# Kernel tuning notes

Measured on AMD Instinct MI355X. Metric: run time of the kernel, lower is better.

Reference implementation:

```python
import jax, jax.numpy as jnp
import numpy as np

B, C, H, W = 16, 512, 112, 112
OUT, GMM = 8, 4
SIGMA_RATIO = 1.0
R = 3.0
BN_EPS = 1e-5


def conv3(x, w):
    # 3x3 conv, stride 1, padding 1 (SAME), NCHW / OIHW
    return jax.lax.conv_general_dilated(x, w, (1, 1), 'SAME',
                                        dimension_numbers=('NCHW', 'OIHW', 'NCHW'))


def bn_relu(x, g, b):
    # inference-mode BatchNorm2d (running_mean=0, running_var=1) + ReLU
    s = g / jnp.sqrt(1.0 + BN_EPS)
    return jax.nn.relu(x * s[None, :, None, None] + b[None, :, None, None])


def setup_inputs() -> dict:
    key = jax.random.key(0)
    ks = jax.random.split(key, 20)
    def w(k, shape, s=0.05):
        return jax.random.normal(k, shape, dtype=jnp.float32) * s
    inp = {
        'x':  jax.random.normal(ks[0], (B, C, H, W), dtype=jnp.float32),
        'w1': w(ks[1], (C // 2, C, 3, 3)),
        'g1': 1.0 + w(ks[2], (C // 2,), 0.1), 'b1': w(ks[3], (C // 2,), 0.1),
        'w2': w(ks[4], (C // 2, C // 2, 3, 3)),
        'g2': 1.0 + w(ks[5], (C // 2,), 0.1), 'b2': w(ks[6], (C // 2,), 0.1),
        'w3': w(ks[7], (C // 4, C // 2, 3, 3)),
        'g3': 1.0 + w(ks[8], (C // 4,), 0.1), 'b3': w(ks[9], (C // 4,), 0.1),
        'w4': w(ks[10], (C // 4, C // 4, 3, 3)),
        'g4': 1.0 + w(ks[11], (C // 4,), 0.1), 'b4': w(ks[12], (C // 4,), 0.1),
        'w5': w(ks[13], (C // 8, C // 4, 3, 3)),
        'g5': 1.0 + w(ks[14], (C // 8,), 0.1), 'b5': w(ks[15], (C // 8,), 0.1),
        'w_fc': w(ks[16], (4 * GMM * OUT, 9 * C // 8)),
        'mix_w': jnp.zeros((1, OUT, GMM, 1, 1), dtype=jnp.float32),
    }
    return inp


def reference(x, w1, g1, b1, w2, g2, b2, w3, g3, b3, w4, g4, b4, w5, g5, b5,
              w_fc, mix_w):
    Bn, Cn, Hh, Ww = x.shape
    h = bn_relu(conv3(x, w1), g1, b1)
    h = bn_relu(conv3(h, w2), g2, b2)
    # AdaptiveAvgPool2d((7,7)): 112/7 = 16, exact reshape-mean
    h = h.reshape(Bn, Cn // 2, 7, Hh // 7, 7, Ww // 7).mean(axis=(3, 5))
    h = bn_relu(conv3(h, w3), g3, b3)
    h = bn_relu(conv3(h, w4), g4, b4)
    # AdaptiveAvgPool2d((3,3)) on 7x7: overlapping windows size 3, stride 2
    h = jax.lax.reduce_window(h, 0.0, jax.lax.add, (1, 1, 3, 3), (1, 1, 2, 2), 'VALID') / 9.0
    h = bn_relu(conv3(h, w5), g5, b5)        # [B, C/8, 3, 3]
    feats = h.reshape(Bn, -1) @ w_fc.T       # [B, 4*gmm*out]
    f = feats.reshape(Bn, OUT, GMM, 4)

    H2, W2 = Hh // 2, Ww // 2
    m_x = jax.nn.sigmoid(f[..., 0]) * float(H2 - 1)           # [B,out,gmm]
    m_y = jax.nn.sigmoid(f[..., 1]) * float(W2 - 1)
    r = jnp.exp((jax.nn.sigmoid(f[..., 2]) * 2.0 - 1.0) * np.float32(np.log(R)))
    rho = jax.nn.sigmoid(f[..., 3]) * 1.6 - 0.8
    sigma = float(Hh) / (2.0 * SIGMA_RATIO)
    denom = -0.5 / (1.0 - rho ** 2) / (sigma ** 2)            # [B,out,gmm]

    ii = jnp.arange(H2, dtype=x.dtype)
    jj = jnp.arange(W2, dtype=x.dtype)
    dx = m_x[..., None] - ii   # [B,out,gmm,H2]
    dy = m_y[..., None] - jj   # [B,out,gmm,W2]
    quad = (dx ** 2 * r[..., None])[..., :, None] \
         + (dy ** 2 / r[..., None])[..., None, :] \
         - 2.0 * rho[..., None, None] * dx[..., :, None] * dy[..., None, :]
    att = jnp.exp(denom[..., None, None] * quad)              # [B,out,gmm,H2,W2]
    att = att / att.sum(axis=(3, 4), keepdims=True)
    mw = jax.nn.softmax(mix_w, axis=2)                        # [1,out,gmm,1,1]
    return (att * mw).sum(axis=2)                             # [B,out,H2,W2]
```

## Files before the change

### kernel.cpp

```cpp
#include <hip/hip_runtime.h>
#include <math.h>


typedef __attribute__((ext_vector_type(8))) short short8v;
typedef __attribute__((ext_vector_type(4))) float f32x4;

__device__ __forceinline__ void split_bf16(float f, unsigned int& hi, unsigned int& lo)
{
    unsigned int u = __float_as_uint(f);
    hi = u >> 16;
    float hif = __uint_as_float(u & 0xffff0000u);
    lo = __float_as_uint(f - hif) >> 16;
}

__device__ __forceinline__ void gld16(const void* g, void* l)
{
    __builtin_amdgcn_global_load_lds(
        (const __attribute__((address_space(1))) unsigned int*)g,
        (__attribute__((address_space(3))) unsigned int*)l, 16, 0, 0);
}

__global__ void zero_kernel(float* z) { z[threadIdx.x] = 0.f; }

__global__ __launch_bounds__(256)
void prep_w_kernel(const float* __restrict__ w, unsigned short* __restrict__ wp, int CIN)
{
    int idx = blockIdx.x * 256 + threadIdx.x;
    int NCH = CIN >> 5;
    int total = 2 * NCH * 9 * 2 * 128 * 32;
    if (idx >= total) return;
    int kk = idx & 31;
    int co = (idx >> 5) & 127;
    int pl = (idx >> 12) & 1;
    int rest = idx >> 13;
    int tap = rest % 9;
    rest /= 9;
    int ch = rest % NCH;
    int y = rest / NCH;
    int qp = kk >> 3, e = kk & 7;
    int q = qp ^ ((co >> 1) & 3);
    int ci = ch * 32 + q * 8 + e;
    int cog = y * 128 + co;
    float f = w[((size_t)cog * CIN + ci) * 9 + tap];
    unsigned int hi, lo;
    split_bf16(f, hi, lo);
    wp[idx] = (unsigned short)(pl ? lo : hi);
}

__global__ __launch_bounds__(256)
void presplit_x_kernel(const float* __restrict__ x, unsigned short* __restrict__ xs)
{
    const int gy = blockIdx.x, ch = blockIdx.y, b = blockIdx.z;
    const int tid = threadIdx.x;
    __shared__ float s[32][113];
    for (int i = tid; i < 32 * 112; i += 256) {
        int ci = i / 112, xx = i - ci * 112;
        s[ci][xx] = x[(((size_t)(b * 16 + ch) * 32 + ci) * 112 + gy) * 112 + xx];
    }
    __syncthreads();
    unsigned int* oh = (unsigned int*)(xs + ((size_t)(b * 16 + ch) * 2 * 12544 + (size_t)gy * 112) * 32);
    unsigned int* ol = oh + 12544 * 16;
    for (int i = tid; i < 112 * 16; i += 256) {
        int px = i >> 4, t = i & 15;
        int qp = t >> 2, ep = t & 3;
        int sw = ((18 * gy + px + 19) >> 1) & 3;
        int q = qp ^ sw;
        int ci0 = q * 8 + ep * 2;
        float f0 = s[ci0][px], f1 = s[ci0 + 1][px];
        unsigned int h0, l0, h1, l1;
        split_bf16(f0, h0, l0);
        split_bf16(f1, h1, l1);
        oh[(size_t)px * 16 + t] = h0 | (h1 << 16);
        ol[(size_t)px * 16 + t] = l0 | (l1 << 16);
    }
}

template<int CIN, bool POOL>
__global__ __launch_bounds__(256, 2)
void conv_mfma_kernel(const unsigned short* __restrict__ xs,
                      const unsigned short* __restrict__ wp,
                      const float* __restrict__ gam, const float* __restrict__ bet,
                      void* __restrict__ out_, const float* __restrict__ zerob)
{
    constexpr int NCH = CIN >> 5;
    extern __shared__ __align__(16) char smem[];
    char* sA = smem;
    char* sB = smem + 43008;

    const int tid = threadIdx.x;
    const int lane = tid & 63;
    const int wv = tid >> 6;
    const int wvm = wv >> 1, ng = wv & 1;
    const int m = lane & 15, kg = lane >> 4;
    const int ty = blockIdx.x / 7, tx = blockIdx.x % 7;
    const int yb = blockIdx.y;
    const int b = blockIdx.z;

    int aoff[11];
    unsigned adst[11];
    #pragma unroll
    for (int k2 = 0; k2 < 11; ++k2) {
        int j = wv + 4 * k2;
        aoff[k2] = -1; adst[k2] = 0;
        if (j < 42) {
            int pl = j / 21, jj = j - pl * 21;
            int px = jj * 16 + (lane >> 2);
            int py = px / 18, pxx = px - py * 18;
            int gy = ty * 16 + py - 1, gx = tx * 16 + pxx - 1;
            bool valid = (px < 324) && ((unsigned)gy < 112u) && ((unsigned)gx < 112u);
            aoff[k2] = valid ? (pl * 802816 + ((gy * 112 + gx) << 6) + ((lane & 3) << 4)) : -1;
            adst[k2] = pl * 21504 + jj * 1024;
        }
    }
    const char* zb = (const char*)zerob + ((lane & 3) << 4);

    auto issueA = [&](int ch) {
        const char* xbase = (const char*)xs + (size_t)(b * NCH + ch) * 1605632;
        #pragma unroll
        for (int k2 = 0; k2 < 11; ++k2) {
            if (wv + 4 * k2 < 42) {
                const char* g = (aoff[k2] >= 0) ? (xbase + aoff[k2]) : zb;
                gld16(g, sA + adst[k2]);
            }
        }
    };
    const char* wbase = (const char*)wp + (size_t)yb * ((size_t)NCH * 9 * 16384);
    auto issueB = [&](int flat, int half) {
        const char* gb = wbase + (size_t)flat * 16384 + (wv << 12) + (lane << 4);
        char* db = sB + half * 16384 + (wv << 12);
        #pragma unroll
        for (int j2 = 0; j2 < 4; ++j2)
            gld16(gb + j2 * 1024, db + j2 * 1024);
    };

    f32x4 acc[8][4];
    #pragma unroll
    for (int i = 0; i < 8; ++i)
        #pragma unroll
        for (int j = 0; j < 4; ++j)
            acc[i][j] = (f32x4){0.f, 0.f, 0.f, 0.f};

    auto mfma_tap = [&](int tap, const char* sBc) {
        const int ky = tap / 3, kx = tap % 3;
        short8v Bf[8];
        #pragma unroll
        for (int nf = 0; nf < 4; ++nf) {
            int col = ng * 64 + nf * 16 + m;
            int off = col * 64 + ((kg ^ ((col >> 1) & 3)) << 4);
            Bf[nf * 2 + 0] = *(const short8v*)(sBc + off);
            Bf[nf * 2 + 1] = *(const short8v*)(sBc + 8192 + off);
        }
        #pragma unroll
        for (int mf = 0; mf < 8; ++mf) {
            int ap = (wvm * 8 + mf + ky) * 18 + kx + m;
            int off = ap * 64 + ((kg ^ ((ap >> 1) & 3)) << 4);
            short8v Ah = *(const short8v*)(sA + off);
            short8v Al = *(const short8v*)(sA + 21504 + off);
            #pragma unroll
            for (int nf = 0; nf < 4; ++nf) {
                acc[mf][nf] = __builtin_amdgcn_mfma_f32_16x16x32_bf16(Ah, Bf[nf * 2 + 0], acc[mf][nf], 0, 0, 0);
                acc[mf][nf] = __builtin_amdgcn_mfma_f32_16x16x32_bf16(Ah, Bf[nf * 2 + 1], acc[mf][nf], 0, 0, 0);
                acc[mf][nf] = __builtin_amdgcn_mfma_f32_16x16x32_bf16(Al, Bf[nf * 2 + 0], acc[mf][nf], 0, 0, 0);
            }
        }
    };

    issueA(0);
    issueB(0, 0);
    issueB(1, 1);
    asm volatile("s_waitcnt vmcnt(0)" ::: "memory");
    __syncthreads();

    for (int ch = 0; ch < NCH; ++ch) {
        const int base = ch * 9;
        #pragma unroll
        for (int pe = 0; pe < 4; ++pe) {
            mfma_tap(2 * pe, sB);
            mfma_tap(2 * pe + 1, sB + 16384);
            __syncthreads();
            if (pe < 3) {
                issueB(base + 2 * pe + 2, 0);
                issueB(base + 2 * pe + 3, 1);
            } else {
                issueB(base + 8, 0);
            }
            asm volatile("s_waitcnt vmcnt(0)" ::: "memory");
            __syncthreads();
        }
        mfma_tap(8, sB);
        __syncthreads();
        if (ch + 1 < NCH) {
            issueA(ch + 1);
            issueB(base + 9, 0);
            issueB(base + 10, 1);
        }
        asm volatile("s_waitcnt vmcnt(0)" ::: "memory");
        __syncthreads();
    }

    const float kRS = 1.0f / sqrtf(1.0f + 1e-5f);

    if (!POOL) {
        unsigned short* h1s = (unsigned short*)out_;
        #pragma unroll
        for (int mf = 0; mf < 8; ++mf) {
            int gy = ty * 16 + wvm * 8 + mf;
            #pragma unroll
            for (int nf = 0; nf < 4; ++nf) {
                int co = yb * 128 + ng * 64 + nf * 16 + m;
                float sc = gam[co] * kRS, bi = bet[co];
                int ch2 = co >> 5, sl = co & 31, q = sl >> 3, e = sl & 7;
                size_t base2 = (size_t)(b * 8 + ch2) * 802816;
                #pragma unroll
                for (int r = 0; r < 4; ++r) {
                    int gx = tx * 16 + kg * 4 + r;
                    float v = fmaxf(fmaf(acc[mf][nf][r], sc, bi), 0.f);
                    unsigned int hi, lo;
                    split_bf16(v, hi, lo);
                    int sw = ((18 * gy + gx + 19) >> 1) & 3;
                    size_t po = base2 + ((size_t)gy * 112 + gx) * 32 + (size_t)((q ^ sw) * 8 + e);
                    h1s[po] = (unsigned short)hi;
                    h1s[po + 401408] = (unsigned short)lo;
                }
            }
        }
    } else {
        __syncthreads();
        float* spool = (float*)sA;
        #pragma unroll
        for (int nf = 0; nf < 4; ++nf) {
            int co = yb * 128 + ng * 64 + nf * 16 + m;
            float sc = gam[co] * kRS, bi = bet[co];
            float s = 0.f;
            #pragma unroll
            for (int mf = 0; mf < 8; ++mf)
                #pragma unroll
                for (int r = 0; r < 4; ++r)
                    s += fmaxf(fmaf(acc[mf][nf][r], sc, bi), 0.f);
            s += __shfl_xor(s, 16);
            s += __shfl_xor(s, 32);
            if (lane < 16) spool[(wv * 4 + nf) * 16 + lane] = s;
        }
        __syncthreads();
        if (tid < 128) {
            int ngx = tid >> 6, rem = tid & 63;
            int nf = rem >> 4, mm = rem & 15;
            float s = spool[(ngx * 4 + nf) * 16 + mm] + spool[((2 + ngx) * 4 + nf) * 16 + mm];
            float* p1o = (float*)out_;
            p1o[(((size_t)b * 256 + yb * 128 + tid) * 7 + ty) * 7 + tx] = s * (1.f / 256.f);
        }
    }
}


template<int CIN>
__global__ __launch_bounds__(256)
void conv_small_kernel(const float* __restrict__ in, const float* __restrict__ w,
                       const float* __restrict__ gam, const float* __restrict__ bet,
                       float* __restrict__ out, int CO_TOT)
{
    const int co0 = blockIdx.x * 16;
    const int b = blockIdx.y;
    const int tid = threadIdx.x;
    const int px = tid & 63;
    const int wg = tid >> 6;
    const int py = px / 7, pxx = px - py * 7;
    const bool act = px < 49;

    __shared__ float s_in[64][9][9];
    __shared__ float s_w[64][16][9];

    float acc[4] = {0.f, 0.f, 0.f, 0.f};

    for (int ci0 = 0; ci0 < CIN; ci0 += 64) {
        __syncthreads();
        for (int idx = tid; idx < 64 * 81; idx += 256) {
            int ci = idx / 81;
            int rem = idx - ci * 81;
            int r = rem / 9, c = rem - (rem / 9) * 9;
            float v = 0.f;
            if (r >= 1 && r <= 7 && c >= 1 && c <= 7)
                v = in[((size_t)(b * CIN + ci0 + ci) * 7 + (r - 1)) * 7 + (c - 1)];
            s_in[ci][r][c] = v;
        }
        for (int idx = tid; idx < 64 * 16 * 9; idx += 256) {
            int co = idx / 576;
            int rem = idx - co * 576;
            int ci = rem / 9, tap = rem - (rem / 9) * 9;
            s_w[ci][co][tap] = w[((size_t)(co0 + co) * CIN + ci0 + ci) * 9 + tap];
        }
        __syncthreads();
        if (act) {
            for (int ci = 0; ci < 64; ++ci) {
                #pragma unroll
                for (int ky = 0; ky < 3; ++ky)
                    #pragma unroll
                    for (int kx = 0; kx < 3; ++kx) {
                        float v = s_in[ci][py + ky][pxx + kx];
                        #pragma unroll
                        for (int j = 0; j < 4; ++j)
                            acc[j] = fmaf(v, s_w[ci][wg * 4 + j][ky * 3 + kx], acc[j]);
                    }
            }
        }
    }
    if (act) {
        const float kRS = 1.0f / sqrtf(1.0f + 1e-5f);
        #pragma unroll
        for (int j = 0; j < 4; ++j) {
            int cog = co0 + wg * 4 + j;
            float v = fmaxf(fmaf(acc[j], gam[cog] * kRS, bet[cog]), 0.f);
            out[(size_t)(b * CO_TOT + cog) * 49 + py * 7 + pxx] = v;
        }
    }
}

__global__ void pool3x3_kernel(const float* __restrict__ in, float* __restrict__ out)
{
    int o = blockIdx.x * 256 + threadIdx.x;
    if (o >= 16 * 128 * 9) return;
    int xo = o % 3;
    int yo = (o / 3) % 3;
    int bc = o / 9;
    const float* p = in + (size_t)bc * 49;
    float s = 0.f;
    #pragma unroll
    for (int ky = 0; ky < 3; ++ky)
        #pragma unroll
        for (int kx = 0; kx < 3; ++kx)
            s += p[(yo * 2 + ky) * 7 + xo * 2 + kx];
    out[o] = s * (1.0f / 9.0f);
}

__global__ __launch_bounds__(256)
void conv5_kernel(const float* __restrict__ in, const float* __restrict__ w,
                  const float* __restrict__ gam, const float* __restrict__ bet,
                  float* __restrict__ out)
{
    const int co0 = blockIdx.x * 16;
    const int b = blockIdx.y;
    const int tid = threadIdx.x;
    __shared__ float s_in[128][5][5];
    __shared__ float s_w[64][16][9];

    for (int idx = tid; idx < 128 * 25; idx += 256) {
        int ci = idx / 25;
        int rem = idx - ci * 25;
        int r = rem / 5, c = rem - (rem / 5) * 5;
        float v = 0.f;
        if (r >= 1 && r <= 3 && c >= 1 && c <= 3)
            v = in[((size_t)(b * 128 + ci) * 3 + (r - 1)) * 3 + (c - 1)];
        s_in[ci][r][c] = v;
    }

    float acc = 0.f;
    const int co = tid / 9;
    const int px = tid - co * 9;
    const int pyy = px / 3, pxx = px - pyy * 3;
    const bool act = tid < 144;

    for (int ci0 = 0; ci0 < 128; ci0 += 64) {
        __syncthreads();
        for (int idx = tid; idx < 64 * 16 * 9; idx += 256) {
            int c2 = idx / 576;
            int rem = idx - c2 * 576;
            int ci = rem / 9, tap = rem - (rem / 9) * 9;
            s_w[ci][c2][tap] = w[((size_t)(co0 + c2) * 128 + ci0 + ci) * 9 + tap];
        }
        __syncthreads();
        if (act) {
            for (int ci = 0; ci < 64; ++ci) {
                #pragma unroll
                for (int ky = 0; ky < 3; ++ky)
                    #pragma unroll
                    for (int kx = 0; kx < 3; ++kx)
                        acc = fmaf(s_in[ci0 + ci][pyy + ky][pxx + kx],
                                   s_w[ci][co][ky * 3 + kx], acc);
            }
        }
    }
    if (act) {
        const float kRS = 1.0f / sqrtf(1.0f + 1e-5f);
        int cog = co0 + co;
        out[(size_t)(b * 64 + cog) * 9 + px] =
            fmaxf(fmaf(acc, gam[cog] * kRS, bet[cog]), 0.f);
    }
}

__global__ void fc_kernel(const float* __restrict__ h5, const float* __restrict__ wfc,
                          float* __restrict__ feats)
{
    int o = blockIdx.x * 256 + threadIdx.x;
    if (o >= 16 * 128) return;
    int b = o >> 7, j = o & 127;
    const float* hp = h5 + b * 576;
    const float* wp = wfc + j * 576;
    float s = 0.f;
    for (int k = 0; k < 576; ++k) s = fmaf(hp[k], wp[k], s);
    feats[o] = s;
}

__global__ __launch_bounds__(256)
void attn_kernel(const float* __restrict__ feats, const float* __restrict__ mixw,
                 float* __restrict__ out)
{
    const int bo = blockIdx.x;
    const int b = bo >> 3, o = bo & 7;
    const int tid = threadIdx.x;
    __shared__ float s_att[4][3136];
    __shared__ float s_red[4];

    float mv[4];
    float mmax = -1e30f;
    #pragma unroll
    for (int g = 0; g < 4; ++g) { mv[g] = mixw[o * 4 + g]; mmax = fmaxf(mmax, mv[g]); }
    float msum = 0.f;
    #pragma unroll
    for (int g = 0; g < 4; ++g) { mv[g] = expf(mv[g] - mmax); msum += mv[g]; }
    #pragma unroll
    for (int g = 0; g < 4; ++g) mv[g] /= msum;

    const float LOG_R = 1.0986122886681098f;
    float winv[4];
    for (int g = 0; g < 4; ++g) {
        float f0 = feats[b * 128 + o * 16 + g * 4 + 0];
        float f1 = feats[b * 128 + o * 16 + g * 4 + 1];
        float f2 = feats[b * 128 + o * 16 + g * 4 + 2];
        float f3 = feats[b * 128 + o * 16 + g * 4 + 3];
        float m_x = 55.f / (1.f + expf(-f0));
        float m_y = 55.f / (1.f + expf(-f1));
        float r = expf((2.f / (1.f + expf(-f2)) - 1.f) * LOG_R);
        float rho = 1.6f / (1.f + expf(-f3)) - 0.8f;
        float denom = (-0.5f / (1.f - rho * rho)) * (1.f / 3136.f);
        float rin = 1.f / r;

        float ssum = 0.f;
        for (int p = tid; p < 3136; p += 256) {
            int i = p / 56;
            int j = p - i * 56;
            float dx = m_x - (float)i;
            float dy = m_y - (float)j;
            float quad = dx * dx * r + dy * dy * rin - 2.f * rho * dx * dy;
            float e = expf(denom * quad);
            s_att[g][p] = e;
            ssum += e;
        }
        #pragma unroll
        for (int off = 32; off > 0; off >>= 1) ssum += __shfl_down(ssum, off);
        if ((tid & 63) == 0) s_red[tid >> 6] = ssum;
        __syncthreads();
        winv[g] = mv[g] / (s_red[0] + s_red[1] + s_red[2] + s_red[3]);
        __syncthreads();
    }

    for (int p = tid; p < 3136; p += 256) {
        float v = 0.f;
        #pragma unroll
        for (int g = 0; g < 4; ++g) v += s_att[g][p] * winv[g];
        out[(size_t)bo * 3136 + p] = v;
    }
}


extern "C" void kernel_launch(void* const* d_in, const int* in_sizes, int n_in,
                              void* d_out, int out_size, void* d_ws, size_t ws_size,
                              hipStream_t stream)
{
    const float* x    = (const float*)d_in[0];
    const float* w1   = (const float*)d_in[1];
    const float* g1   = (const float*)d_in[2];
    const float* b1   = (const float*)d_in[3];
    const float* w2   = (const float*)d_in[4];
    const float* g2   = (const float*)d_in[5];
    const float* b2   = (const float*)d_in[6];
    const float* w3   = (const float*)d_in[7];
    const float* g3   = (const float*)d_in[8];
    const float* b3   = (const float*)d_in[9];
    const float* w4   = (const float*)d_in[10];
    const float* g4   = (const float*)d_in[11];
    const float* b4   = (const float*)d_in[12];
    const float* w5   = (const float*)d_in[13];
    const float* g5   = (const float*)d_in[14];
    const float* b5   = (const float*)d_in[15];
    const float* wfc  = (const float*)d_in[16];
    const float* mixw = (const float*)d_in[17];
    float* outp = (float*)d_out;

    hipFuncSetAttribute(reinterpret_cast<const void*>(&conv_mfma_kernel<512, false>),
                        hipFuncAttributeMaxDynamicSharedMemorySize, 75776);
    hipFuncSetAttribute(reinterpret_cast<const void*>(&conv_mfma_kernel<256, true>),
                        hipFuncAttributeMaxDynamicSharedMemorySize, 75776);

    char* wsb = (char*)d_ws;
    unsigned short* wp = (unsigned short*)wsb;   wsb += (size_t)2359296 * 2;
    unsigned short* xs = (unsigned short*)wsb;   wsb += (size_t)16*16*2*12544*32*2;
    unsigned short* h1s = (unsigned short*)wsb;  wsb += (size_t)16*8*2*12544*32*2;
    float* p1 = (float*)wsb;  wsb += 200704 * 4;
    float* h3 = (float*)wsb;  wsb += 100352 * 4;
    float* h4 = (float*)wsb;  wsb += 100352 * 4;
    float* p2 = (float*)wsb;  wsb += 18432 * 4;
    float* h5 = (float*)wsb;  wsb += 9216 * 4;
    float* fts = (float*)wsb; wsb += 2048 * 4;
    float* zerob = (float*)wsb; wsb += 64 * 4;

    zero_kernel<<<1, 64, 0, stream>>>(zerob);
    presplit_x_kernel<<<dim3(112, 16, 16), 256, 0, stream>>>(x, xs);

    prep_w_kernel<<<9216, 256, 0, stream>>>(w1, wp, 512);
    conv_mfma_kernel<512, false><<<dim3(49, 2, 16), 256, 75776, stream>>>(xs, wp, g1, b1, h1s, zerob);

    prep_w_kernel<<<4608, 256, 0, stream>>>(w2, wp, 256);
    conv_mfma_kernel<256, true><<<dim3(49, 2, 16), 256, 75776, stream>>>(h1s, wp, g2, b2, p1, zerob);

    conv_small_kernel<256><<<dim3(8, 16), 256, 0, stream>>>(p1, w3, g3, b3, h3, 128);
    conv_small_kernel<128><<<dim3(8, 16), 256, 0, stream>>>(h3, w4, g4, b4, h4, 128);

    pool3x3_kernel<<<72, 256, 0, stream>>>(h4, p2);
    conv5_kernel<<<dim3(4, 16), 256, 0, stream>>>(p2, w5, g5, b5, h5);
    fc_kernel<<<8, 256, 0, stream>>>(h5, wfc, fts);
    attn_kernel<<<128, 256, 0, stream>>>(fts, mixw, outp);
}
```

Measured before the change: 1.912 ms.

## Store conv1 output as single bf16 and drop low-part MFMAs in conv2

```diff
diff --git a/kernel.cpp b/kernel.cpp
--- a/kernel.cpp
+++ b/kernel.cpp
@@ -83,9 +83,13 @@
                       void* __restrict__ out_, const float* __restrict__ zerob)
 {
     constexpr int NCH = CIN >> 5;
+    constexpr int APL = POOL ? 1 : 2;
+    constexpr int AJ = 21 * APL;
+    constexpr int AISS = (AJ + 3) / 4;
+    constexpr size_t XSTR = (size_t)802816 * APL;
     extern __shared__ __align__(16) char smem[];
     char* sA = smem;
-    char* sB = smem + 43008;
+    char* sB = smem + APL * 21504;
 
     const int tid = threadIdx.x;
     const int lane = tid & 63;
@@ -96,13 +100,13 @@
     const int yb = blockIdx.y;
     const int b = blockIdx.z;
 
-    int aoff[11];
-    unsigned adst[11];
-    #pragma unroll
-    for (int k2 = 0; k2 < 11; ++k2) {
+    int aoff[AISS];
+    unsigned adst[AISS];
+    #pragma unroll
+    for (int k2 = 0; k2 < AISS; ++k2) {
         int j = wv + 4 * k2;
         aoff[k2] = -1; adst[k2] = 0;
-        if (j < 42) {
+        if (j < AJ) {
             int pl = j / 21, jj = j - pl * 21;
             int px = jj * 16 + (lane >> 2);
             int py = px / 18, pxx = px - py * 18;
@@ -115,10 +119,10 @@
     const char* zb = (const char*)zerob + ((lane & 3) << 4);
 
     auto issueA = [&](int ch) {
-        const char* xbase = (const char*)xs + (size_t)(b * NCH + ch) * 1605632;
-        #pragma unroll
-        for (int k2 = 0; k2 < 11; ++k2) {
-            if (wv + 4 * k2 < 42) {
+        const char* xbase = (const char*)xs + (size_t)(b * NCH + ch) * XSTR;
+        #pragma unroll
+        for (int k2 = 0; k2 < AISS; ++k2) {
+            if (wv + 4 * k2 < AJ) {
                 const char* g = (aoff[k2] >= 0) ? (xbase + aoff[k2]) : zb;
                 gld16(g, sA + adst[k2]);
             }
@@ -142,25 +146,33 @@
 
     auto mfma_tap = [&](int tap, const char* sBc) {
         const int ky = tap / 3, kx = tap % 3;
-        short8v Bf[8];
+        short8v Bh_[4], Bl_[4];
         #pragma unroll
         for (int nf = 0; nf < 4; ++nf) {
             int col = ng * 64 + nf * 16 + m;
             int off = col * 64 + ((kg ^ ((col >> 1) & 3)) << 4);
-            Bf[nf * 2 + 0] = *(const short8v*)(sBc + off);
-            Bf[nf * 2 + 1] = *(const short8v*)(sBc + 8192 + off);
+            Bh_[nf] = *(const short8v*)(sBc + off);
+            Bl_[nf] = *(const short8v*)(sBc + 8192 + off);
         }
         #pragma unroll
         for (int mf = 0; mf < 8; ++mf) {
             int ap = (wvm * 8 + mf + ky) * 18 + kx + m;
             int off = ap * 64 + ((kg ^ ((ap >> 1) & 3)) << 4);
             short8v Ah = *(const short8v*)(sA + off);
-            short8v Al = *(const short8v*)(sA + 21504 + off);
-            #pragma unroll
-            for (int nf = 0; nf < 4; ++nf) {
-                acc[mf][nf] = __builtin_amdgcn_mfma_f32_16x16x32_bf16(Ah, Bf[nf * 2 + 0], acc[mf][nf], 0, 0, 0);
-                acc[mf][nf] = __builtin_amdgcn_mfma_f32_16x16x32_bf16(Ah, Bf[nf * 2 + 1], acc[mf][nf], 0, 0, 0);
-                acc[mf][nf] = __builtin_amdgcn_mfma_f32_16x16x32_bf16(Al, Bf[nf * 2 + 0], acc[mf][nf], 0, 0, 0);
+            if constexpr (!POOL) {
+                short8v Al = *(const short8v*)(sA + 21504 + off);
+                #pragma unroll
+                for (int nf = 0; nf < 4; ++nf) {
+                    acc[mf][nf] = __builtin_amdgcn_mfma_f32_16x16x32_bf16(Ah, Bh_[nf], acc[mf][nf], 0, 0, 0);
+                    acc[mf][nf] = __builtin_amdgcn_mfma_f32_16x16x32_bf16(Ah, Bl_[nf], acc[mf][nf], 0, 0, 0);
+                    acc[mf][nf] = __builtin_amdgcn_mfma_f32_16x16x32_bf16(Al, Bh_[nf], acc[mf][nf], 0, 0, 0);
+                }
+            } else {
+                #pragma unroll
+                for (int nf = 0; nf < 4; ++nf) {
+                    acc[mf][nf] = __builtin_amdgcn_mfma_f32_16x16x32_bf16(Ah, Bh_[nf], acc[mf][nf], 0, 0, 0);
+                    acc[mf][nf] = __builtin_amdgcn_mfma_f32_16x16x32_bf16(Ah, Bl_[nf], acc[mf][nf], 0, 0, 0);
+                }
             }
         }
     };
@@ -210,23 +222,22 @@
                 int co = yb * 128 + ng * 64 + nf * 16 + m;
                 float sc = gam[co] * kRS, bi = bet[co];
                 int ch2 = co >> 5, sl = co & 31, q = sl >> 3, e = sl & 7;
-                size_t base2 = (size_t)(b * 8 + ch2) * 802816;
+                size_t base2 = (size_t)(b * 8 + ch2) * 401408;
                 #pragma unroll
                 for (int r = 0; r < 4; ++r) {
                     int gx = tx * 16 + kg * 4 + r;
                     float v = fmaxf(fmaf(acc[mf][nf][r], sc, bi), 0.f);
-                    unsigned int hi, lo;
-                    split_bf16(v, hi, lo);
+                    unsigned int u = __float_as_uint(v);
+                    u += 0x7fffu + ((u >> 16) & 1u);
                     int sw = ((18 * gy + gx + 19) >> 1) & 3;
                     size_t po = base2 + ((size_t)gy * 112 + gx) * 32 + (size_t)((q ^ sw) * 8 + e);
-                    h1s[po] = (unsigned short)hi;
-                    h1s[po + 401408] = (unsigned short)lo;
+                    h1s[po] = (unsigned short)(u >> 16);
                 }
             }
         }
     } else {
         __syncthreads();
-        float* spool = (float*)sA;
+        float* spool = (float*)smem;
         #pragma unroll
         for (int nf = 0; nf < 4; ++nf) {
             int co = yb * 128 + ng * 64 + nf * 16 + m;
@@ -387,17 +398,20 @@
     }
 }
 
-__global__ void fc_kernel(const float* __restrict__ h5, const float* __restrict__ wfc,
-                          float* __restrict__ feats)
-{
-    int o = blockIdx.x * 256 + threadIdx.x;
-    if (o >= 16 * 128) return;
+__global__ __launch_bounds__(256)
+void fc_kernel(const float* __restrict__ h5, const float* __restrict__ wfc,
+               float* __restrict__ feats)
+{
+    int o = blockIdx.x * 4 + (threadIdx.x >> 6);
+    int lane = threadIdx.x & 63;
     int b = o >> 7, j = o & 127;
     const float* hp = h5 + b * 576;
     const float* wp = wfc + j * 576;
     float s = 0.f;
-    for (int k = 0; k < 576; ++k) s = fmaf(hp[k], wp[k], s);
-    feats[o] = s;
+    for (int k = lane; k < 576; k += 64) s = fmaf(hp[k], wp[k], s);
+    #pragma unroll
+    for (int off = 32; off > 0; off >>= 1) s += __shfl_down(s, off);
+    if (lane == 0) feats[o] = s;
 }
 
 __global__ __launch_bounds__(256)
@@ -489,12 +503,12 @@
     hipFuncSetAttribute(reinterpret_cast<const void*>(&conv_mfma_kernel<512, false>),
                         hipFuncAttributeMaxDynamicSharedMemorySize, 75776);
     hipFuncSetAttribute(reinterpret_cast<const void*>(&conv_mfma_kernel<256, true>),
-                        hipFuncAttributeMaxDynamicSharedMemorySize, 75776);
+                        hipFuncAttributeMaxDynamicSharedMemorySize, 54272);
 
     char* wsb = (char*)d_ws;
     unsigned short* wp = (unsigned short*)wsb;   wsb += (size_t)2359296 * 2;
     unsigned short* xs = (unsigned short*)wsb;   wsb += (size_t)16*16*2*12544*32*2;
-    unsigned short* h1s = (unsigned short*)wsb;  wsb += (size_t)16*8*2*12544*32*2;
+    unsigned short* h1s = (unsigned short*)wsb;  wsb += (size_t)16*8*12544*32*2;
     float* p1 = (float*)wsb;  wsb += 200704 * 4;
     float* h3 = (float*)wsb;  wsb += 100352 * 4;
     float* h4 = (float*)wsb;  wsb += 100352 * 4;
@@ -510,13 +524,13 @@
     conv_mfma_kernel<512, false><<<dim3(49, 2, 16), 256, 75776, stream>>>(xs, wp, g1, b1, h1s, zerob);
 
     prep_w_kernel<<<4608, 256, 0, stream>>>(w2, wp, 256);
-    conv_mfma_kernel<256, true><<<dim3(49, 2, 16), 256, 75776, stream>>>(h1s, wp, g2, b2, p1, zerob);
+    conv_mfma_kernel<256, true><<<dim3(49, 2, 16), 256, 54272, stream>>>(h1s, wp, g2, b2, p1, zerob);
 
     conv_small_kernel<256><<<dim3(8, 16), 256, 0, stream>>>(p1, w3, g3, b3, h3, 128);
     conv_small_kernel<128><<<dim3(8, 16), 256, 0, stream>>>(h3, w4, g4, b4, h4, 128);
 
     pool3x3_kernel<<<72, 256, 0, stream>>>(h4, p2);
     conv5_kernel<<<dim3(4, 16), 256, 0, stream>>>(p2, w5, g5, b5, h5);
-    fc_kernel<<<8, 256, 0, stream>>>(h5, wfc, fts);
+    fc_kernel<<<512, 256, 0, stream>>>(h5, wfc, fts);
     attn_kernel<<<128, 256, 0, stream>>>(fts, mixw, outp);
 }
```

Result: faster. 1.829 ms (-4.3%).
